# Kernel optimization log

Measured on AMD Instinct MI355X. Metric: run time of the kernel, lower is better.

The kernel has to match this reference:

```python
import jax, jax.numpy as jnp
import numpy as np

DIM = 1024
HEADS = 16
DIM_HEAD = DIM // HEADS  # 64
B, N = 4, 1024


def setup_inputs() -> dict:
    key = jax.random.key(0)
    ks = jax.random.split(key, 8)
    s = 1.0 / np.sqrt(DIM)
    inp = {
        "x": jax.random.normal(ks[0], (B, N, DIM), dtype=jnp.float32),
        # weights stored as [in, out] so y = x @ W (+ b), equivalent to torch Linear
        "Wq": jax.random.normal(ks[1], (DIM, DIM), dtype=jnp.float32) * s,
        "Wk": jax.random.normal(ks[2], (DIM, DIM), dtype=jnp.float32) * s,
        "Wv": jax.random.normal(ks[3], (DIM, DIM), dtype=jnp.float32) * s,
        "Wproj": jax.random.normal(ks[4], (DIM, DIM), dtype=jnp.float32) * s,
        "bproj": jnp.zeros((DIM,), dtype=jnp.float32),
        "Wpre": jax.random.normal(ks[5], (DIM, DIM), dtype=jnp.float32) * s,
        "bpre": jnp.zeros((DIM,), dtype=jnp.float32),
        # original init is -inf (non-runnable); use a finite trained value
        "pi": jnp.full((1,), 0.5, dtype=jnp.float32),
    }
    return inp


def reference(x, Wq, Wk, Wv, Wproj, bproj, Wpre, bpre, pi):
    b, n, c = x.shape
    h, dh = HEADS, DIM_HEAD
    residual = x
    # bias-logit path: Linear -> SiLU -> bmm with itself (dropout p=0 is identity)
    pre = jax.nn.silu(x @ Wpre + bpre)                       # [B,N,C]
    logits = jnp.einsum('bnc,bmc->bnm', pre, pre) / jnp.sqrt(jnp.float32(c))
    # QKV (x2 defaults to x)
    q = (x @ Wq).reshape(b, n, h, dh).transpose(0, 2, 1, 3)  # [B,H,N,Dh]
    k = (x @ Wk).reshape(b, n, h, dh).transpose(0, 2, 1, 3)
    v = (x @ Wv).reshape(b, n, h, dh).transpose(0, 2, 1, 3)
    score = jnp.einsum('bhnd,bhmd->bhnm', q, k) / jnp.sqrt(jnp.float32(dh))
    final_logits = pi[0] * logits[:, None, :, :] + score     # broadcast bias over heads
    attn = jax.nn.softmax(final_logits, axis=-1)
    out = jnp.einsum('bhnm,bhmd->bhnd', attn, v)             # [B,H,N,Dh]
    out = out.transpose(0, 2, 1, 3).reshape(b, n, h * dh)
    out = out @ Wproj + bproj
    return out + residual
```

## Files before the change

### kernel.cpp

```cpp
#include <hip/hip_runtime.h>

using bf16x8 = __attribute__((ext_vector_type(8))) short;
using v8bf   = __attribute__((ext_vector_type(8))) __bf16;
using f32x4  = __attribute__((ext_vector_type(4))) float;
using u32x2  = __attribute__((ext_vector_type(2))) unsigned;
using bf16x2 = __attribute__((ext_vector_type(2))) __bf16;

typedef const __attribute__((address_space(1))) void GASV;
typedef __attribute__((address_space(3))) void LASV;

template <typename V>
__device__ __forceinline__ auto mfma_bf16_impl(V a, V b, f32x4 c, int)
    -> decltype(__builtin_amdgcn_mfma_f32_16x16x32_bf16(a, b, c, 0, 0, 0)) {
  return __builtin_amdgcn_mfma_f32_16x16x32_bf16(a, b, c, 0, 0, 0);
}
template <typename V>
__device__ __forceinline__ f32x4 mfma_bf16_impl(V a, V b, f32x4 c, long) {
  return __builtin_amdgcn_mfma_f32_16x16x32_bf16(
      __builtin_bit_cast(v8bf, a), __builtin_bit_cast(v8bf, b), c, 0, 0, 0);
}
__device__ __forceinline__ f32x4 MFMA(bf16x8 a, bf16x8 b, f32x4 c) {
  return mfma_bf16_impl(a, b, c, 0);
}

__device__ __forceinline__ void async_lds16(const void* g, void* l) {
  __builtin_amdgcn_global_load_lds((GASV*)g, (LASV*)l, 16, 0, 0);
}

__device__ __forceinline__ unsigned short f2bf(float x) {
  unsigned u = __float_as_uint(x);
  u = u + 0x7fffu + ((u >> 16) & 1u);
  return (unsigned short)(u >> 16);
}

__device__ __forceinline__ unsigned pack_bf2(float lo, float hi) {
  bf16x2 t;
  t[0] = (__bf16)lo;
  t[1] = (__bf16)hi;
  return __builtin_bit_cast(unsigned, t);
}

#define LOG2E 1.4426950408889634f
#define SOFT_OFF 14.0f

__global__ __launch_bounds__(256) void k_prep(
    const float4* __restrict__ x, ushort4* __restrict__ xb,
    const float* __restrict__ w0, const float* __restrict__ w1,
    const float* __restrict__ w2, const float* __restrict__ w3,
    const float* __restrict__ w4, unsigned short* __restrict__ out) {
  const int bid = blockIdx.x, tid = threadIdx.x;
  if (bid < 4096) {
    const int i = bid * 256 + tid;
    float4 v = x[i];
    ushort4 p;
    p.x = f2bf(v.x); p.y = f2bf(v.y); p.z = f2bf(v.z); p.w = f2bf(v.w);
    xb[i] = p;
    return;
  }
  __shared__ float t[32][33];
  const int tb = bid - 4096;
  const int z = tb >> 10;
  const float* W = (z == 0) ? w0 : (z == 1) ? w1 : (z == 2) ? w2 : (z == 3) ? w3 : w4;
  const float sc = (z == 1) ? (LOG2E / 8.0f) : 1.0f;
  unsigned short* o = out + (size_t)z * (1u << 20);
  const int bx = (tb & 31) * 32, by = ((tb >> 5) & 31) * 32;
  const int tx = tid & 31, ty = tid >> 5;
#pragma unroll
  for (int i = 0; i < 4; ++i)
    t[ty + i * 8][tx] = W[(size_t)(by + ty + i * 8) * 1024 + bx + tx];
  __syncthreads();
#pragma unroll
  for (int i = 0; i < 4; ++i)
    o[(size_t)(bx + ty + i * 8) * 1024 + by + tx] = f2bf(t[tx][ty + i * 8] * sc);
}

template <int MI, int NI>
__device__ __forceinline__ void gemm_core_t(const unsigned short* __restrict__ A,
                                            const unsigned short* __restrict__ Bt,
                                            unsigned short* ldsA,
                                            unsigned short* ldsB,
                                            f32x4 acc[MI][NI]) {
  const int tid = threadIdx.x;
  const int w = tid >> 6, lane = tid & 63;
  const int lane15 = lane & 15, quad = lane >> 4;
  const int wm = w >> 1, wn = w & 1;
  for (int ko = 0; ko < 16; ++ko) {
    __syncthreads();
#pragma unroll
    for (int i = 0; i < MI; ++i) {
      const int p = i * 256 + tid;
      const int r = p >> 3, cc = (p & 7) ^ (r & 7);
      async_lds16(A + r * 1024 + ko * 64 + cc * 8, ldsA + (i * 256 + w * 64) * 8);
    }
#pragma unroll
    for (int i = 0; i < NI; ++i) {
      const int p = i * 256 + tid;
      const int r = p >> 3, cc = (p & 7) ^ (r & 7);
      async_lds16(Bt + r * 1024 + ko * 64 + cc * 8, ldsB + (i * 256 + w * 64) * 8);
    }
    __syncthreads();
    bf16x8 af[MI][2], bfr[NI][2];
#pragma unroll
    for (int t = 0; t < MI; ++t) {
      const int row = wm * (MI * 16) + t * 16 + lane15;
#pragma unroll
      for (int h = 0; h < 2; ++h)
        af[t][h] = *(const bf16x8*)&ldsA[row * 64 + (((h * 4 + quad) ^ (row & 7)) << 3)];
    }
#pragma unroll
    for (int t = 0; t < NI; ++t) {
      const int row = wn * (NI * 16) + t * 16 + lane15;
#pragma unroll
      for (int h = 0; h < 2; ++h)
        bfr[t][h] = *(const bf16x8*)&ldsB[row * 64 + (((h * 4 + quad) ^ (row & 7)) << 3)];
    }
#pragma unroll
    for (int mi = 0; mi < MI; ++mi)
#pragma unroll
      for (int ni = 0; ni < NI; ++ni) {
        acc[mi][ni] = MFMA(af[mi][0], bfr[ni][0], acc[mi][ni]);
        acc[mi][ni] = MFMA(af[mi][1], bfr[ni][1], acc[mi][ni]);
      }
  }
}

#define GEMM_PROLOGUE(MI_, NI_)                                      \
  __shared__ unsigned short ldsA[(MI_)*32 * 64];                     \
  __shared__ unsigned short ldsB[(NI_)*32 * 64];                     \
  f32x4 acc[MI_][NI_];                                               \
  {                                                                  \
    f32x4 z_ = {0.f, 0.f, 0.f, 0.f};                                 \
    for (int i_ = 0; i_ < (MI_); ++i_)                               \
      for (int j_ = 0; j_ < (NI_); ++j_) acc[i_][j_] = z_;           \
  }

#define GEMM_EPI_IDX(MI_, NI_)                                       \
  const int tid = threadIdx.x, w = tid >> 6, lane = tid & 63;        \
  const int lane15 = lane & 15, quad = lane >> 4;                    \
  const int wm = w >> 1, wn = w & 1;                                 \
  const int r0 = tm + wm * ((MI_)*16) + quad * 4;                    \
  const int c0 = tn + wn * ((NI_)*16) + lane15;

__global__ __launch_bounds__(512, 2) void k_gemm_qkvpre(
    const unsigned short* __restrict__ xb, const unsigned short* __restrict__ wt,
    const float* __restrict__ bpre, unsigned short* __restrict__ pre,
    unsigned short* __restrict__ qb, unsigned short* __restrict__ kb,
    unsigned short* __restrict__ vt) {
  __shared__ unsigned short ldsA[2][256 * 64];
  __shared__ unsigned short ldsB[2][256 * 64];
  const int bid = blockIdx.x;
  const int xcd = bid & 7, idx = bid >> 3;
  const int z = xcd >> 1, half = xcd & 1;
  const int wtile = (idx >> 3) * 256;
  const int stile = half * 2048 + (idx & 7) * 256;
  int tm, tn;
  if (z == 3) { tm = stile; tn = wtile; }
  else        { tm = wtile; tn = stile; }
  const unsigned short* At =
      (z == 3) ? xb + (size_t)tm * 1024
               : wt + (size_t)z * (1u << 20) + (size_t)tm * 1024;
  const unsigned short* Bt_ =
      (z == 3) ? wt + (size_t)3 * (1u << 20) + (size_t)tn * 1024
               : xb + (size_t)tn * 1024;

  const int tid = threadIdx.x, w = tid >> 6, lane = tid & 63;
  const int lane15 = lane & 15, quad = lane >> 4;
  const int wm = w >> 2, wn = w & 3;

  f32x4 acc[8][4];
  {
    f32x4 z_ = {0.f, 0.f, 0.f, 0.f};
#pragma unroll
    for (int i = 0; i < 8; ++i)
#pragma unroll
      for (int j = 0; j < 4; ++j) acc[i][j] = z_;
  }

  auto stage = [&](int ko, int buf) {
#pragma unroll
    for (int j = 0; j < 4; ++j) {
      const int p = j * 512 + tid;
      const int r = p >> 3, cc = (p & 7) ^ (r & 7);
      async_lds16(At + (size_t)r * 1024 + ko * 64 + cc * 8,
                  &ldsA[buf][(j * 512 + w * 64) * 8]);
      async_lds16(Bt_ + (size_t)r * 1024 + ko * 64 + cc * 8,
                  &ldsB[buf][(j * 512 + w * 64) * 8]);
    }
  };

  auto compute = [&](int buf) {
    const unsigned short* sA = ldsA[buf];
    const unsigned short* sB = ldsB[buf];
    bf16x8 bfr[4][2];
#pragma unroll
    for (int nf = 0; nf < 4; ++nf) {
      const int row = wn * 64 + nf * 16 + lane15;
#pragma unroll
      for (int kh = 0; kh < 2; ++kh)
        bfr[nf][kh] =
            *(const bf16x8*)&sB[row * 64 + (((kh * 4 + quad) ^ (row & 7)) << 3)];
    }
#pragma unroll
    for (int mp = 0; mp < 4; ++mp) {
      bf16x8 af[2][2];
#pragma unroll
      for (int i = 0; i < 2; ++i) {
        const int row = wm * 128 + (mp * 2 + i) * 16 + lane15;
#pragma unroll
        for (int kh = 0; kh < 2; ++kh)
          af[i][kh] =
              *(const bf16x8*)&sA[row * 64 + (((kh * 4 + quad) ^ (row & 7)) << 3)];
      }
      __builtin_amdgcn_s_setprio(1);
#pragma unroll
      for (int i = 0; i < 2; ++i)
#pragma unroll
        for (int nf = 0; nf < 4; ++nf) {
          acc[mp * 2 + i][nf] = MFMA(af[i][0], bfr[nf][0], acc[mp * 2 + i][nf]);
          acc[mp * 2 + i][nf] = MFMA(af[i][1], bfr[nf][1], acc[mp * 2 + i][nf]);
        }
      __builtin_amdgcn_s_setprio(0);
    }
  };

  stage(0, 0);
  __syncthreads();
  for (int t = 0; t < 16; ++t) {
    if (t + 1 < 16) stage(t + 1, (t + 1) & 1);
    compute(t & 1);
    __syncthreads();
  }

  const int r0 = tm + wm * 128 + quad * 4;
  const int c0 = tn + wn * 64 + lane15;
  if (z == 0) {
#pragma unroll
    for (int mf = 0; mf < 8; ++mf) {
      const float4 b4 = *(const float4*)&bpre[r0 + mf * 16];
#pragma unroll
      for (int nf = 0; nf < 4; ++nf) {
        const int seq = c0 + nf * 16;
        float vv[4];
#pragma unroll
        for (int rr = 0; rr < 4; ++rr) {
          float v = acc[mf][nf][rr] + ((const float*)&b4)[rr];
          vv[rr] = v / (1.0f + __expf(-v));
        }
        ushort4 pk;
        pk.x = f2bf(vv[0]); pk.y = f2bf(vv[1]);
        pk.z = f2bf(vv[2]); pk.w = f2bf(vv[3]);
        *(ushort4*)&pre[(size_t)seq * 1024 + r0 + mf * 16] = pk;
      }
    }
  } else if (z == 1 || z == 2) {
    unsigned short* dst = (z == 1) ? qb : kb;
#pragma unroll
    for (int mf = 0; mf < 8; ++mf)
#pragma unroll
      for (int nf = 0; nf < 4; ++nf) {
        const int seq = c0 + nf * 16;
        ushort4 pk;
        pk.x = f2bf(acc[mf][nf][0]); pk.y = f2bf(acc[mf][nf][1]);
        pk.z = f2bf(acc[mf][nf][2]); pk.w = f2bf(acc[mf][nf][3]);
        *(ushort4*)&dst[(size_t)seq * 1024 + r0 + mf * 16] = pk;
      }
  } else {
#pragma unroll
    for (int mf = 0; mf < 8; ++mf) {
      const int m = r0 + mf * 16;
      const int bb_ = m >> 10, nseq = m & 1023;
#pragma unroll
      for (int nf = 0; nf < 4; ++nf) {
        const int cg = c0 + nf * 16;
        const int hh = cg >> 6, dd = cg & 63;
        ushort4 pk;
        pk.x = f2bf(acc[mf][nf][0]); pk.y = f2bf(acc[mf][nf][1]);
        pk.z = f2bf(acc[mf][nf][2]); pk.w = f2bf(acc[mf][nf][3]);
        *(ushort4*)&vt[(size_t)(((bb_ * 16 + hh) << 6) + dd) * 1024 + nseq] = pk;
      }
    }
  }
}

__global__ __launch_bounds__(256) void k_gemm_logits(
    const unsigned short* __restrict__ pre, const float* __restrict__ pi,
    unsigned short* __restrict__ lg) {
  const int bz = blockIdx.z;
  const unsigned short* base = pre + ((size_t)bz << 20);
  const int tm = blockIdx.y * 64, tn = blockIdx.x * 128;
  GEMM_PROLOGUE(2, 4);
  gemm_core_t<2, 4>(base + (size_t)tm * 1024, base + (size_t)tn * 1024, ldsA, ldsB, acc);
  const float sc = pi[0] * (LOG2E / 32.0f);
  GEMM_EPI_IDX(2, 4);
#pragma unroll
  for (int mi = 0; mi < 2; ++mi)
#pragma unroll
    for (int ni = 0; ni < 4; ++ni) {
      const int col = c0 + ni * 16;
      ushort4 pk;
      pk.x = f2bf(acc[mi][ni][0] * sc); pk.y = f2bf(acc[mi][ni][1] * sc);
      pk.z = f2bf(acc[mi][ni][2] * sc); pk.w = f2bf(acc[mi][ni][3] * sc);
      *(ushort4*)&lg[((size_t)bz << 20) + (size_t)col * 1024 + r0 + mi * 16] = pk;
    }
}

__global__ __launch_bounds__(256) void k_gemm_out(
    const unsigned short* __restrict__ ao, const unsigned short* __restrict__ wtp,
    const float* __restrict__ bproj, const float* __restrict__ xres,
    float* __restrict__ out) {
  const int tm = blockIdx.x * 64, tn = blockIdx.y * 128;
  GEMM_PROLOGUE(2, 4);
  gemm_core_t<2, 4>(wtp + (size_t)tm * 1024, ao + (size_t)tn * 1024, ldsA, ldsB, acc);
  GEMM_EPI_IDX(2, 4);
#pragma unroll
  for (int mi = 0; mi < 2; ++mi) {
    const float4 b4 = *(const float4*)&bproj[r0 + mi * 16];
#pragma unroll
    for (int ni = 0; ni < 4; ++ni) {
      const int seq = c0 + ni * 16;
      const size_t idx = (size_t)seq * 1024 + r0 + mi * 16;
      const float4 rv = *(const float4*)&xres[idx];
      float4 ov;
      ov.x = acc[mi][ni][0] + b4.x + rv.x;
      ov.y = acc[mi][ni][1] + b4.y + rv.y;
      ov.z = acc[mi][ni][2] + b4.z + rv.z;
      ov.w = acc[mi][ni][3] + b4.w + rv.w;
      *(float4*)&out[idx] = ov;
    }
  }
}

__global__ __launch_bounds__(256, 4) void k_attn(
    const unsigned short* __restrict__ qb, const unsigned short* __restrict__ kb,
    const unsigned short* __restrict__ vt, const unsigned short* __restrict__ lg,
    unsigned short* __restrict__ ao) {
  __shared__ unsigned short ldsK[2 * 64 * 64];
  __shared__ unsigned short ldsV[2 * 64 * 64];
  const int bid = blockIdx.x;
  const int xcd = bid & 7, idx = bid >> 3;
  const int b = xcd >> 1, hg = xcd & 1;
  const int h = hg * 8 + (idx >> 4);
  const int q0 = (idx & 15) * 64;
  const int tid = threadIdx.x, w = tid >> 6, lane = tid & 63;
  const int lane15 = lane & 15, quad = lane >> 4;
  const int qw = q0 + w * 16;

  bf16x8 qf[2];
  {
    const unsigned short* qrow =
        qb + (size_t)((b << 10) + qw + lane15) * 1024 + (h << 6);
    qf[0] = *(const bf16x8*)(qrow + quad * 8);
    qf[1] = *(const bf16x8*)(qrow + 32 + quad * 8);
  }
  const unsigned short* kbase = kb + ((size_t)(b << 10)) * 1024 + (h << 6);
  const unsigned short* vbase = vt + ((size_t)((b * 16 + h) << 6)) * 1024;
  const unsigned short* lgrow =
      lg + ((size_t)b << 20) + (size_t)(qw + lane15) * 1024 +
      (quad >> 1) * 16 + (quad & 1) * 4;

  float lcol = 0.f;
  f32x4 o[4];
  {
    f32x4 z_ = {0.f, 0.f, 0.f, 0.f};
#pragma unroll
    for (int nt = 0; nt < 4; ++nt) o[nt] = z_;
  }

  uint2 lgc[4], lgn[4];

  auto stage = [&](int ch, unsigned short* sK, unsigned short* sV) {
    const int kv0 = ch * 64;
#pragma unroll
    for (int i = 0; i < 2; ++i) {
      const int p = i * 256 + tid;
      const int r = p >> 3, cc = (p & 7) ^ (r & 7);
      const int rk = (r & 0x27) | ((r & 8) << 1) | ((r & 16) >> 1);
      async_lds16(kbase + (size_t)(kv0 + rk) * 1024 + cc * 8,
                  sK + (i * 256 + w * 64) * 8);
      async_lds16(vbase + (size_t)r * 1024 + kv0 + cc * 8,
                  sV + (i * 256 + w * 64) * 8);
    }
  };
  auto lgload = [&](int ch, uint2 dst[4]) {
#pragma unroll
    for (int mi = 0; mi < 4; ++mi)
      dst[mi] = *(const uint2*)(lgrow + ch * 64 + (mi >> 1) * 32 + (mi & 1) * 8);
  };
  auto compute = [&](const unsigned short* sK, const unsigned short* sV) {
    f32x4 s[4];
    __builtin_amdgcn_s_setprio(1);
#pragma unroll
    for (int mi = 0; mi < 4; ++mi) {
      const int row = mi * 16 + lane15;
      bf16x8 k0 = *(const bf16x8*)&sK[row * 64 + ((quad ^ (row & 7)) << 3)];
      bf16x8 k1 = *(const bf16x8*)&sK[row * 64 + (((4 + quad) ^ (row & 7)) << 3)];
      f32x4 t;
      t[0] = __uint_as_float(lgc[mi].x << 16);
      t[1] = __uint_as_float(lgc[mi].x & 0xffff0000u);
      t[2] = __uint_as_float(lgc[mi].y << 16);
      t[3] = __uint_as_float(lgc[mi].y & 0xffff0000u);
      t = MFMA(k0, qf[0], t);
      t = MFMA(k1, qf[1], t);
      s[mi] = t;
    }
    __builtin_amdgcn_s_setprio(0);
    float rs = 0.f;
    uint2 pk[4];
#pragma unroll
    for (int mi = 0; mi < 4; ++mi) {
      const float p0 = __builtin_amdgcn_exp2f(s[mi][0] - SOFT_OFF);
      const float p1 = __builtin_amdgcn_exp2f(s[mi][1] - SOFT_OFF);
      const float p2 = __builtin_amdgcn_exp2f(s[mi][2] - SOFT_OFF);
      const float p3 = __builtin_amdgcn_exp2f(s[mi][3] - SOFT_OFF);
      rs += (p0 + p1) + (p2 + p3);
      pk[mi].x = pack_bf2(p0, p1);
      pk[mi].y = pack_bf2(p2, p3);
    }
    lcol += rs;

#pragma unroll
    for (int kp = 0; kp < 2; ++kp) {
      u32x2 rx = __builtin_amdgcn_permlane16_swap(pk[2 * kp].x, pk[2 * kp + 1].x, 0, 0);
      u32x2 ry = __builtin_amdgcn_permlane16_swap(pk[2 * kp].y, pk[2 * kp + 1].y, 0, 0);
      uint4 bfv;
      bfv.x = rx.x;
      bfv.y = ry.x;
      bfv.z = rx.y;
      bfv.w = ry.y;
      const bf16x8 pf = __builtin_bit_cast(bf16x8, bfv);
      __builtin_amdgcn_s_setprio(1);
#pragma unroll
      for (int dt = 0; dt < 4; ++dt) {
        const int d = dt * 16 + lane15;
        bf16x8 vf = *(const bf16x8*)&sV[d * 64 +
                                        (((kp * 4 + quad) ^ (d & 7)) << 3)];
        o[dt] = MFMA(vf, pf, o[dt]);
      }
      __builtin_amdgcn_s_setprio(0);
    }
  };

  unsigned short* sK0 = ldsK;
  unsigned short* sK1 = ldsK + 64 * 64;
  unsigned short* sV0 = ldsV;
  unsigned short* sV1 = ldsV + 64 * 64;

  stage(0, sK0, sV0);
  lgload(0, lgc);
  __syncthreads();

  for (int c = 0; c < 16; c += 2) {
    stage(c + 1, sK1, sV1);
    lgload(c + 1, lgn);
    compute(sK0, sV0);
    __syncthreads();
#pragma unroll
    for (int mi = 0; mi < 4; ++mi) lgc[mi] = lgn[mi];
    if (c + 2 < 16) {
      stage(c + 2, sK0, sV0);
      lgload(c + 2, lgn);
    }
    compute(sK1, sV1);
    __syncthreads();
#pragma unroll
    for (int mi = 0; mi < 4; ++mi) lgc[mi] = lgn[mi];
  }

  lcol += __shfl_xor(lcol, 16);
  lcol += __shfl_xor(lcol, 32);
  const float rinv = 1.0f / lcol;
  const int m = (b << 10) + qw + lane15;
#pragma unroll
  for (int dt = 0; dt < 4; ++dt) {
    ushort4 pkk;
    pkk.x = f2bf(o[dt][0] * rinv);
    pkk.y = f2bf(o[dt][1] * rinv);
    pkk.z = f2bf(o[dt][2] * rinv);
    pkk.w = f2bf(o[dt][3] * rinv);
    *(ushort4*)&ao[(size_t)m * 1024 + (h << 6) + dt * 16 + quad * 4] = pkk;
  }
}

extern "C" void kernel_launch(void* const* d_in, const int* in_sizes, int n_in,
                              void* d_out, int out_size, void* d_ws, size_t ws_size,
                              hipStream_t stream) {
  const float* x     = (const float*)d_in[0];
  const float* Wq    = (const float*)d_in[1];
  const float* Wk    = (const float*)d_in[2];
  const float* Wv    = (const float*)d_in[3];
  const float* Wproj = (const float*)d_in[4];
  const float* bproj = (const float*)d_in[5];
  const float* Wpre  = (const float*)d_in[6];
  const float* bpre  = (const float*)d_in[7];
  const float* pi    = (const float*)d_in[8];
  float* out = (float*)d_out;
  char* ws = (char*)d_ws;

  unsigned short* xb  = (unsigned short*)(ws);
  unsigned short* wt  = (unsigned short*)(ws + (8u << 20));
  unsigned short* pre = (unsigned short*)(ws + (18u << 20));
  unsigned short* qb  = (unsigned short*)(ws + (26u << 20));
  unsigned short* kb  = (unsigned short*)(ws + (34u << 20));
  unsigned short* vt  = (unsigned short*)(ws + (42u << 20));
  unsigned short* lg  = xb;
  unsigned short* ao  = pre;

  k_prep<<<dim3(4096 + 5120), dim3(256), 0, stream>>>(
      (const float4*)x, (ushort4*)xb, Wpre, Wq, Wk, Wv, Wproj, wt);
  k_gemm_qkvpre<<<dim3(256), dim3(512), 0, stream>>>(xb, wt, bpre, pre, qb, kb, vt);
  k_gemm_logits<<<dim3(8, 16, 4), dim3(256), 0, stream>>>(pre, pi, lg);
  k_attn<<<dim3(1024), dim3(256), 0, stream>>>(qb, kb, vt, lg, ao);
  k_gemm_out<<<dim3(16, 32, 1), dim3(256), 0, stream>>>(ao, wt + 4 * (1u << 20), bproj, x, out);
}
```

Baseline: 212.4 us.

## Split GEMM k-step into four barrier-separated MFMA quadrants with staggered prefetch

Restructures the projection GEMM main loop into a ping-pong style schedule. A and B fragments are read in halves, and the next tile's global-to-LDS loads are issued separately for A and B between compute phases. Explicit s_barrier, lgkmcnt and vmcnt waits replace __syncthreads. The aim is to overlap LDS reads and global prefetch with MFMA work and to let waves interleave. The cost is many more barriers per k-step and possible stalls from vmcnt(0) waits.

```diff
diff --git a/kernel.cpp b/kernel.cpp
--- a/kernel.cpp
+++ b/kernel.cpp
@@ -42,6 +42,14 @@
 
 #define LOG2E 1.4426950408889634f
 #define SOFT_OFF 14.0f
+
+#define BAR() __builtin_amdgcn_s_barrier()
+#define WAIT_LGKM0()                                           \
+  do {                                                         \
+    asm volatile("s_waitcnt lgkmcnt(0)" ::: "memory");         \
+    __builtin_amdgcn_sched_barrier(0);                         \
+  } while (0)
+#define WAIT_VM0() asm volatile("s_waitcnt vmcnt(0)" ::: "memory")
 
 __global__ __launch_bounds__(256) void k_prep(
     const float4* __restrict__ x, ushort4* __restrict__ xb,
@@ -176,59 +184,90 @@
       for (int j = 0; j < 4; ++j) acc[i][j] = z_;
   }
 
-  auto stage = [&](int ko, int buf) {
+  auto stageA = [&](int ko, int buf) {
 #pragma unroll
     for (int j = 0; j < 4; ++j) {
       const int p = j * 512 + tid;
       const int r = p >> 3, cc = (p & 7) ^ (r & 7);
       async_lds16(At + (size_t)r * 1024 + ko * 64 + cc * 8,
                   &ldsA[buf][(j * 512 + w * 64) * 8]);
+    }
+  };
+  auto stageB = [&](int ko, int buf) {
+#pragma unroll
+    for (int j = 0; j < 4; ++j) {
+      const int p = j * 512 + tid;
+      const int r = p >> 3, cc = (p & 7) ^ (r & 7);
       async_lds16(Bt_ + (size_t)r * 1024 + ko * 64 + cc * 8,
                   &ldsB[buf][(j * 512 + w * 64) * 8]);
     }
   };
 
-  auto compute = [&](int buf) {
+  bf16x8 af[4][2], bn0[2][2], bn1[2][2];
+  auto rdA = [&](const unsigned short* sA, int msub) {
+#pragma unroll
+    for (int i = 0; i < 4; ++i) {
+      const int row = wm * 128 + (msub * 4 + i) * 16 + lane15;
+#pragma unroll
+      for (int kh = 0; kh < 2; ++kh)
+        af[i][kh] =
+            *(const bf16x8*)&sA[row * 64 + (((kh * 4 + quad) ^ (row & 7)) << 3)];
+    }
+  };
+  auto rdB = [&](const unsigned short* sB, int nsub, bf16x8 bf2[2][2]) {
+#pragma unroll
+    for (int i = 0; i < 2; ++i) {
+      const int row = wn * 64 + (nsub * 2 + i) * 16 + lane15;
+#pragma unroll
+      for (int kh = 0; kh < 2; ++kh)
+        bf2[i][kh] =
+            *(const bf16x8*)&sB[row * 64 + (((kh * 4 + quad) ^ (row & 7)) << 3)];
+    }
+  };
+  auto quad16 = [&](bf16x8 bf2[2][2], int mo, int no) {
+    __builtin_amdgcn_s_setprio(1);
+#pragma unroll
+    for (int i = 0; i < 4; ++i)
+#pragma unroll
+      for (int j = 0; j < 2; ++j) {
+        acc[mo + i][no + j] = MFMA(af[i][0], bf2[j][0], acc[mo + i][no + j]);
+        acc[mo + i][no + j] = MFMA(af[i][1], bf2[j][1], acc[mo + i][no + j]);
+      }
+    __builtin_amdgcn_s_setprio(0);
+  };
+
+  stageA(0, 0);
+  stageB(0, 0);
+  WAIT_VM0();
+  BAR();
+
+  for (int t = 0; t < 16; ++t) {
+    const int buf = t & 1;
     const unsigned short* sA = ldsA[buf];
     const unsigned short* sB = ldsB[buf];
-    bf16x8 bfr[4][2];
-#pragma unroll
-    for (int nf = 0; nf < 4; ++nf) {
-      const int row = wn * 64 + nf * 16 + lane15;
-#pragma unroll
-      for (int kh = 0; kh < 2; ++kh)
-        bfr[nf][kh] =
-            *(const bf16x8*)&sB[row * 64 + (((kh * 4 + quad) ^ (row & 7)) << 3)];
-    }
-#pragma unroll
-    for (int mp = 0; mp < 4; ++mp) {
-      bf16x8 af[2][2];
-#pragma unroll
-      for (int i = 0; i < 2; ++i) {
-        const int row = wm * 128 + (mp * 2 + i) * 16 + lane15;
-#pragma unroll
-        for (int kh = 0; kh < 2; ++kh)
-          af[i][kh] =
-              *(const bf16x8*)&sA[row * 64 + (((kh * 4 + quad) ^ (row & 7)) << 3)];
-      }
-      __builtin_amdgcn_s_setprio(1);
-#pragma unroll
-      for (int i = 0; i < 2; ++i)
-#pragma unroll
-        for (int nf = 0; nf < 4; ++nf) {
-          acc[mp * 2 + i][nf] = MFMA(af[i][0], bfr[nf][0], acc[mp * 2 + i][nf]);
-          acc[mp * 2 + i][nf] = MFMA(af[i][1], bfr[nf][1], acc[mp * 2 + i][nf]);
-        }
-      __builtin_amdgcn_s_setprio(0);
-    }
-  };
-
-  stage(0, 0);
-  __syncthreads();
-  for (int t = 0; t < 16; ++t) {
-    if (t + 1 < 16) stage(t + 1, (t + 1) & 1);
-    compute(t & 1);
-    __syncthreads();
+    const bool pf = (t + 1 < 16);
+    rdA(sA, 0);
+    rdB(sB, 0, bn0);
+    if (pf) stageA(t + 1, buf ^ 1);
+    BAR();
+    WAIT_LGKM0();
+    quad16(bn0, 0, 0);
+    BAR();
+    rdB(sB, 1, bn1);
+    if (pf) stageB(t + 1, buf ^ 1);
+    BAR();
+    WAIT_LGKM0();
+    quad16(bn1, 0, 2);
+    BAR();
+    rdA(sA, 1);
+    BAR();
+    WAIT_LGKM0();
+    quad16(bn0, 4, 0);
+    BAR();
+    WAIT_VM0();
+    BAR();
+    quad16(bn1, 4, 2);
+    BAR();
   }
 
   const int r0 = tm + wm * 128 + quad * 4;
```

After: 211.4 us. No clear change (-0.4%).

## Shrink QKV/pre GEMM tiles to 256x128 with K=32 steps and double the grid

Applied to the files above, without the earlier changes.

The fused QKV/pre projection GEMM moves from 256x256 output tiles with K-step 64 to 256x128 tiles with K-step 32, which halves LDS use. The grid doubles to 512 blocks, launch bounds now request 4 blocks per CU, and the LDS swizzle and the block-to-tile mapping are reworked to match. The aim is more blocks in flight and better latency hiding on a small 256-block grid. In exchange, operands are reused less per tile and there are twice as many sync iterations.

```diff
diff --git a/kernel.cpp b/kernel.cpp
--- a/kernel.cpp
+++ b/kernel.cpp
@@ -141,21 +141,24 @@
   const int r0 = tm + wm * ((MI_)*16) + quad * 4;                    \
   const int c0 = tn + wn * ((NI_)*16) + lane15;
 
-__global__ __launch_bounds__(512, 2) void k_gemm_qkvpre(
+__global__ __launch_bounds__(512, 4) void k_gemm_qkvpre(
     const unsigned short* __restrict__ xb, const unsigned short* __restrict__ wt,
     const float* __restrict__ bpre, unsigned short* __restrict__ pre,
     unsigned short* __restrict__ qb, unsigned short* __restrict__ kb,
     unsigned short* __restrict__ vt) {
-  __shared__ unsigned short ldsA[2][256 * 64];
-  __shared__ unsigned short ldsB[2][256 * 64];
+  __shared__ unsigned short ldsA[2][256 * 32];
+  __shared__ unsigned short ldsB[2][128 * 32];
   const int bid = blockIdx.x;
   const int xcd = bid & 7, idx = bid >> 3;
   const int z = xcd >> 1, half = xcd & 1;
-  const int wtile = (idx >> 3) * 256;
-  const int stile = half * 2048 + (idx & 7) * 256;
   int tm, tn;
-  if (z == 3) { tm = stile; tn = wtile; }
-  else        { tm = wtile; tn = stile; }
+  if (z == 3) {
+    tm = half * 2048 + (idx >> 3) * 256;
+    tn = (idx & 7) * 128;
+  } else {
+    tm = (idx >> 4) * 256;
+    tn = half * 2048 + (idx & 15) * 128;
+  }
   const unsigned short* At =
       (z == 3) ? xb + (size_t)tm * 1024
                : wt + (size_t)z * (1u << 20) + (size_t)tm * 1024;
@@ -165,77 +168,66 @@
 
   const int tid = threadIdx.x, w = tid >> 6, lane = tid & 63;
   const int lane15 = lane & 15, quad = lane >> 4;
-  const int wm = w >> 2, wn = w & 3;
-
-  f32x4 acc[8][4];
+  const int wm = w >> 1, wn = w & 1;
+
+  f32x4 acc[4][4];
   {
     f32x4 z_ = {0.f, 0.f, 0.f, 0.f};
 #pragma unroll
-    for (int i = 0; i < 8; ++i)
+    for (int i = 0; i < 4; ++i)
 #pragma unroll
       for (int j = 0; j < 4; ++j) acc[i][j] = z_;
   }
 
   auto stage = [&](int ko, int buf) {
 #pragma unroll
-    for (int j = 0; j < 4; ++j) {
+    for (int j = 0; j < 2; ++j) {
       const int p = j * 512 + tid;
-      const int r = p >> 3, cc = (p & 7) ^ (r & 7);
-      async_lds16(At + (size_t)r * 1024 + ko * 64 + cc * 8,
+      const int r = p >> 2, cc = (p & 3) ^ ((r >> 1) & 3);
+      async_lds16(At + (size_t)r * 1024 + ko * 32 + cc * 8,
                   &ldsA[buf][(j * 512 + w * 64) * 8]);
-      async_lds16(Bt_ + (size_t)r * 1024 + ko * 64 + cc * 8,
-                  &ldsB[buf][(j * 512 + w * 64) * 8]);
+    }
+    {
+      const int p = tid;
+      const int r = p >> 2, cc = (p & 3) ^ ((r >> 1) & 3);
+      async_lds16(Bt_ + (size_t)r * 1024 + ko * 32 + cc * 8,
+                  &ldsB[buf][(w * 64) * 8]);
     }
   };
 
-  auto compute = [&](int buf) {
+  stage(0, 0);
+  __syncthreads();
+  for (int t = 0; t < 32; ++t) {
+    const int buf = t & 1;
+    if (t + 1 < 32) stage(t + 1, buf ^ 1);
     const unsigned short* sA = ldsA[buf];
     const unsigned short* sB = ldsB[buf];
-    bf16x8 bfr[4][2];
-#pragma unroll
-    for (int nf = 0; nf < 4; ++nf) {
-      const int row = wn * 64 + nf * 16 + lane15;
-#pragma unroll
-      for (int kh = 0; kh < 2; ++kh)
-        bfr[nf][kh] =
-            *(const bf16x8*)&sB[row * 64 + (((kh * 4 + quad) ^ (row & 7)) << 3)];
-    }
-#pragma unroll
-    for (int mp = 0; mp < 4; ++mp) {
-      bf16x8 af[2][2];
-#pragma unroll
-      for (int i = 0; i < 2; ++i) {
-        const int row = wm * 128 + (mp * 2 + i) * 16 + lane15;
-#pragma unroll
-        for (int kh = 0; kh < 2; ++kh)
-          af[i][kh] =
-              *(const bf16x8*)&sA[row * 64 + (((kh * 4 + quad) ^ (row & 7)) << 3)];
-      }
-      __builtin_amdgcn_s_setprio(1);
-#pragma unroll
-      for (int i = 0; i < 2; ++i)
-#pragma unroll
-        for (int nf = 0; nf < 4; ++nf) {
-          acc[mp * 2 + i][nf] = MFMA(af[i][0], bfr[nf][0], acc[mp * 2 + i][nf]);
-          acc[mp * 2 + i][nf] = MFMA(af[i][1], bfr[nf][1], acc[mp * 2 + i][nf]);
-        }
-      __builtin_amdgcn_s_setprio(0);
-    }
-  };
-
-  stage(0, 0);
-  __syncthreads();
-  for (int t = 0; t < 16; ++t) {
-    if (t + 1 < 16) stage(t + 1, (t + 1) & 1);
-    compute(t & 1);
+    bf16x8 af[4], bf[4];
+#pragma unroll
+    for (int mi = 0; mi < 4; ++mi) {
+      const int row = wm * 64 + mi * 16 + lane15;
+      af[mi] = *(const bf16x8*)&sA[row * 32 + ((quad ^ ((row >> 1) & 3)) << 3)];
+    }
+#pragma unroll
+    for (int ni = 0; ni < 4; ++ni) {
+      const int row = wn * 64 + ni * 16 + lane15;
+      bf[ni] = *(const bf16x8*)&sB[row * 32 + ((quad ^ ((row >> 1) & 3)) << 3)];
+    }
+    __builtin_amdgcn_s_setprio(1);
+#pragma unroll
+    for (int mi = 0; mi < 4; ++mi)
+#pragma unroll
+      for (int ni = 0; ni < 4; ++ni)
+        acc[mi][ni] = MFMA(af[mi], bf[ni], acc[mi][ni]);
+    __builtin_amdgcn_s_setprio(0);
     __syncthreads();
   }
 
-  const int r0 = tm + wm * 128 + quad * 4;
+  const int r0 = tm + wm * 64 + quad * 4;
   const int c0 = tn + wn * 64 + lane15;
   if (z == 0) {
 #pragma unroll
-    for (int mf = 0; mf < 8; ++mf) {
+    for (int mf = 0; mf < 4; ++mf) {
       const float4 b4 = *(const float4*)&bpre[r0 + mf * 16];
 #pragma unroll
       for (int nf = 0; nf < 4; ++nf) {
@@ -255,7 +247,7 @@
   } else if (z == 1 || z == 2) {
     unsigned short* dst = (z == 1) ? qb : kb;
 #pragma unroll
-    for (int mf = 0; mf < 8; ++mf)
+    for (int mf = 0; mf < 4; ++mf)
 #pragma unroll
       for (int nf = 0; nf < 4; ++nf) {
         const int seq = c0 + nf * 16;
@@ -266,7 +258,7 @@
       }
   } else {
 #pragma unroll
-    for (int mf = 0; mf < 8; ++mf) {
+    for (int mf = 0; mf < 4; ++mf) {
       const int m = r0 + mf * 16;
       const int bb_ = m >> 10, nseq = m & 1023;
 #pragma unroll
@@ -507,7 +499,7 @@
 
   k_prep<<<dim3(4096 + 5120), dim3(256), 0, stream>>>(
       (const float4*)x, (ushort4*)xb, Wpre, Wq, Wk, Wv, Wproj, wt);
-  k_gemm_qkvpre<<<dim3(256), dim3(512), 0, stream>>>(xb, wt, bpre, pre, qb, kb, vt);
+  k_gemm_qkvpre<<<dim3(512), dim3(512), 0, stream>>>(xb, wt, bpre, pre, qb, kb, vt);
   k_gemm_logits<<<dim3(8, 16, 4), dim3(256), 0, stream>>>(pre, pi, lg);
   k_attn<<<dim3(1024), dim3(256), 0, stream>>>(qb, kb, vt, lg, ao);
   k_gemm_out<<<dim3(16, 32, 1), dim3(256), 0, stream>>>(ao, wt + 4 * (1u << 20), bproj, x, out);
```

After: 210.9 us. No clear change (-0.7%).
